# Optimization experiments

Hardware: AMD Instinct MI355X
Metric: run time of the kernel (lower is better)

Reference implementation:

```python
import jax, jax.numpy as jnp
import numpy as np

HID = 1024
HEADS = 16
HEAD_DIM = HID // HEADS
MLP_HID = 4096
TEMB = 1024
EPS = 1e-6


def _ln(x):
    # LayerNorm without affine, eps=1e-6
    mu = jnp.mean(x, axis=-1, keepdims=True)
    var = jnp.var(x, axis=-1, keepdims=True)
    return (x - mu) * jax.lax.rsqrt(var + EPS)


def _modulate(x, shift, scale):
    return x * (1.0 + scale[:, None, :]) + shift[:, None, :]


def setup_inputs() -> dict:
    key = jax.random.key(0)
    ks = jax.random.split(key, 12)
    s = 0.02
    return {
        "x": jax.random.normal(ks[0], (8, 1024, HID), jnp.float32),
        "c": jax.random.normal(ks[1], (8, TEMB), jnp.float32),
        "W_qkv": jax.random.normal(ks[2], (HID, 3 * HID), jnp.float32) * s,
        "b_qkv": jnp.zeros((3 * HID,), jnp.float32),
        "W_proj": jax.random.normal(ks[3], (HID, HID), jnp.float32) * s,
        "b_proj": jnp.zeros((HID,), jnp.float32),
        "W_fc1": jax.random.normal(ks[4], (HID, MLP_HID), jnp.float32) * s,
        "b_fc1": jnp.zeros((MLP_HID,), jnp.float32),
        "W_fc2": jax.random.normal(ks[5], (MLP_HID, HID), jnp.float32) * s,
        "b_fc2": jnp.zeros((HID,), jnp.float32),
        "W_ada": jax.random.normal(ks[6], (TEMB, 6 * HID), jnp.float32) * s,
        "b_ada": jnp.zeros((6 * HID,), jnp.float32),
    }


def _attn(x, W_qkv, b_qkv, W_proj, b_proj):
    B, N, C = x.shape
    qkv = x @ W_qkv + b_qkv                      # [B,N,3C]
    qkv = qkv.reshape(B, N, 3, HEADS, HEAD_DIM)
    q, k, v = qkv[:, :, 0], qkv[:, :, 1], qkv[:, :, 2]  # [B,N,H,D]
    scale = HEAD_DIM ** -0.5
    logits = jnp.einsum('bnhd,bmhd->bhnm', q, k) * scale
    attn = jax.nn.softmax(logits, axis=-1)
    out = jnp.einsum('bhnm,bmhd->bnhd', attn, v).reshape(B, N, C)
    return out @ W_proj + b_proj


def reference(x, c, W_qkv, b_qkv, W_proj, b_proj, W_fc1, b_fc1, W_fc2, b_fc2, W_ada, b_ada):
    ada = jax.nn.silu(c) @ W_ada + b_ada          # [B,6C]
    shift_msa, scale_msa, gate_msa, shift_mlp, scale_mlp, gate_mlp = jnp.split(ada, 6, axis=1)

    h = _modulate(_ln(x), shift_msa, scale_msa)
    x = x + gate_msa[:, None, :] * _attn(h, W_qkv, b_qkv, W_proj, b_proj)

    h = _modulate(_ln(x), shift_mlp, scale_mlp)
    h = jax.nn.gelu(h @ W_fc1 + b_fc1, approximate=True) @ W_fc2 + b_fc2
    x = x + gate_mlp[:, None, :] * h
    return x
```

## Files before the change

### kernel.cpp

```cpp
#include <hip/hip_runtime.h>
#include <stdint.h>

typedef unsigned short u16;
typedef __attribute__((ext_vector_type(4))) float f32x4;
typedef __attribute__((ext_vector_type(8))) short bf16x8;
typedef bf16x8 bf16x8a __attribute__((may_alias));
typedef uint32_t u32a __attribute__((may_alias));

#define HID 1024
#define MLPD 4096
#define TEMB 1024
#define ADA_N 6144
#define SEQ 1024
#define BATCH 8
#define KCH 32
#define KCHLEN (TEMB / KCH)

__device__ __forceinline__ u16 f2bf_bits(float f) {
  uint32_t u = __float_as_uint(f);
  uint32_t r = (u + 0x7FFFu + ((u >> 16) & 1u)) >> 16;
  return (u16)r;
}

__device__ __forceinline__ uint32_t cvt_pk_bf16(float lo, float hi) {
  uint32_t r;
  asm("v_cvt_pk_bf16_f32 %0, %1, %2" : "=v"(r) : "v"(lo), "v"(hi));
  return r;
}

__device__ __forceinline__ float exp2_hw(float x) {
#if __has_builtin(__builtin_amdgcn_exp2f)
  return __builtin_amdgcn_exp2f(x);
#else
  return exp2f(x);
#endif
}

__device__ __forceinline__ void async_copy16(void* lds_dst, const void* g_src) {
  __builtin_amdgcn_global_load_lds(
      (const __attribute__((address_space(1))) void*)(uintptr_t)g_src,
      (__attribute__((address_space(3))) void*)(uint32_t)(uintptr_t)lds_dst,
      16, 0, 0);
}

__device__ __forceinline__ float gelu_tanh(float v) {
  float u = 0.7978845608028654f * (v + 0.044715f * v * v * v);
  float e = __expf(2.f * u);
  return v * e / (e + 1.f);
}

__global__ __launch_bounds__(256) void transpose_bf16(const float* __restrict__ W,
                                                      u16* __restrict__ Wt, int K, int N) {
  __shared__ float tile[32][33];
  int n0 = blockIdx.x * 32, k0 = blockIdx.y * 32;
  int tx = threadIdx.x & 31, ty = threadIdx.x >> 5;
#pragma unroll
  for (int i = 0; i < 4; i++)
    tile[ty + i * 8][tx] = W[(size_t)(k0 + ty + i * 8) * N + n0 + tx];
  __syncthreads();
#pragma unroll
  for (int i = 0; i < 4; i++)
    Wt[(size_t)(n0 + ty + i * 8) * K + k0 + tx] = f2bf_bits(tile[tx][ty + i * 8]);
}

__global__ __launch_bounds__(256) void ada_part(const float* __restrict__ c,
                                                const float* __restrict__ W,
                                                float* __restrict__ part) {
  __shared__ float sc[BATCH * KCHLEN];
  int t = threadIdx.x;
  int col = blockIdx.x * 256 + t;
  int kc = blockIdx.y;
  int k0 = kc * KCHLEN;
  for (int i = t; i < BATCH * KCHLEN; i += 256) {
    int b = i >> 5, kk = i & (KCHLEN - 1);
    float v = c[b * TEMB + k0 + kk];
    sc[i] = v / (1.f + __expf(-v));
  }
  __syncthreads();
  float acc[BATCH] = {};
  for (int kk = 0; kk < KCHLEN; kk++) {
    float w = W[(size_t)(k0 + kk) * ADA_N + col];
#pragma unroll
    for (int b = 0; b < BATCH; b++) acc[b] += sc[b * KCHLEN + kk] * w;
  }
#pragma unroll
  for (int b = 0; b < BATCH; b++)
    part[((size_t)kc * BATCH + b) * ADA_N + col] = acc[b];
}

__global__ __launch_bounds__(256) void ada_reduce(const float* __restrict__ part,
                                                  const float* __restrict__ bias,
                                                  float* __restrict__ out) {
  int i = blockIdx.x * 256 + threadIdx.x;
  int col = i % ADA_N, b = i / ADA_N;
  float s = bias[col];
#pragma unroll
  for (int kc = 0; kc < KCH; kc++)
    s += part[((size_t)kc * BATCH + b) * ADA_N + col];
  out[(size_t)b * ADA_N + col] = s;
}

__global__ __launch_bounds__(256) void ln_mod(const float* __restrict__ x,
                                              const float* __restrict__ ada,
                                              int shift_off, int scale_off,
                                              u16* __restrict__ h) {
  int row = blockIdx.x;
  int bb = row >> 10;
  int t = threadIdx.x;
  const float4 v = ((const float4*)(x + (size_t)row * HID))[t];
  float s = v.x + v.y + v.z + v.w;
  float sq = v.x * v.x + v.y * v.y + v.z * v.z + v.w * v.w;
#pragma unroll
  for (int off = 32; off >= 1; off >>= 1) {
    s += __shfl_xor(s, off);
    sq += __shfl_xor(sq, off);
  }
  __shared__ float red[8];
  int wid = t >> 6;
  if ((t & 63) == 0) { red[wid] = s; red[4 + wid] = sq; }
  __syncthreads();
  s = red[0] + red[1] + red[2] + red[3];
  sq = red[4] + red[5] + red[6] + red[7];
  float mu = s * (1.0f / HID);
  float rs = rsqrtf(sq * (1.0f / HID) - mu * mu + 1e-6f);
  const float4 sc = ((const float4*)(ada + (size_t)bb * ADA_N + scale_off))[t];
  const float4 sh = ((const float4*)(ada + (size_t)bb * ADA_N + shift_off))[t];
  ushort4 o;
  o.x = f2bf_bits((v.x - mu) * rs * (1.f + sc.x) + sh.x);
  o.y = f2bf_bits((v.y - mu) * rs * (1.f + sc.y) + sh.y);
  o.z = f2bf_bits((v.z - mu) * rs * (1.f + sc.z) + sh.z);
  o.w = f2bf_bits((v.w - mu) * rs * (1.f + sc.w) + sh.w);
  ((ushort4*)(h + (size_t)row * HID))[t] = o;
}

template <int EPI>
__global__ __launch_bounds__(256) void gemm(const u16* __restrict__ A,
                                            const u16* __restrict__ Bt,
                                            const float* __restrict__ bias,
                                            void* __restrict__ Cout,
                                            const float* __restrict__ resid,
                                            const float* __restrict__ gate,
                                            int N, int K) {
  __shared__ u16 As[128 * 32];
  __shared__ u16 Bs[128 * 32];
  int t = threadIdx.x;
  int lane = t & 63, wid = t >> 6;
  int l15 = lane & 15, l4 = lane >> 4;
  int wr = wid >> 1, wc = wid & 1;
  int lid = blockIdx.y * gridDim.x + blockIdx.x;
  int nwg = gridDim.y * gridDim.x;
  int swz = (lid & 7) * (nwg >> 3) + (lid >> 3);
  int nx = gridDim.x;
  int m0 = (swz / nx) * 128, n0 = (swz % nx) * 128;
  f32x4 acc[4][4] = {};
  const u16* Abase = A + (size_t)m0 * K;
  const u16* Bbase = Bt + (size_t)n0 * K;
  for (int k0 = 0; k0 < K; k0 += 32) {
#pragma unroll
    for (int i = 0; i < 2; i++) {
      int idx = i * 256 + t;
      int row = idx >> 2, ch = idx & 3;
      async_copy16(&As[idx * 8], Abase + (size_t)row * K + k0 + ch * 8);
      async_copy16(&Bs[idx * 8], Bbase + (size_t)row * K + k0 + ch * 8);
    }
    asm volatile("s_waitcnt vmcnt(0)" ::: "memory");
    __syncthreads();
    bf16x8 af[4], bfr[4];
#pragma unroll
    for (int mi = 0; mi < 4; mi++)
      af[mi] = *(const bf16x8a*)&As[(wr * 64 + mi * 16 + l15) * 32 + l4 * 8];
#pragma unroll
    for (int ni = 0; ni < 4; ni++)
      bfr[ni] = *(const bf16x8a*)&Bs[(wc * 64 + ni * 16 + l15) * 32 + l4 * 8];
#pragma unroll
    for (int mi = 0; mi < 4; mi++)
#pragma unroll
      for (int ni = 0; ni < 4; ni++)
        acc[mi][ni] = __builtin_amdgcn_mfma_f32_16x16x32_bf16(af[mi], bfr[ni], acc[mi][ni], 0, 0, 0);
    __syncthreads();
  }
  int brow = m0 + wr * 64, bcol = n0 + wc * 64;
  int bb = m0 >> 10;
#pragma unroll
  for (int ni = 0; ni < 4; ni++) {
    int col = bcol + ni * 16 + l15;
    float bv = bias[col];
    float gv = (EPI == 2) ? gate[(size_t)bb * ADA_N + col] : 0.f;
#pragma unroll
    for (int mi = 0; mi < 4; mi++) {
#pragma unroll
      for (int r = 0; r < 4; r++) {
        int row = brow + mi * 16 + l4 * 4 + r;
        float v = acc[mi][ni][r] + bv;
        if (EPI == 0) {
          ((u16*)Cout)[(size_t)row * N + col] = f2bf_bits(v);
        } else if (EPI == 1) {
          ((u16*)Cout)[(size_t)row * N + col] = f2bf_bits(gelu_tanh(v));
        } else {
          ((float*)Cout)[(size_t)row * N + col] =
              resid[(size_t)row * N + col] + gv * v;
        }
      }
    }
  }
}

__global__ __launch_bounds__(256, 3) void attn_kernel(const u16* __restrict__ qkv,
                                                      u16* __restrict__ O) {
  const int KSTR = 72, VSTR = 72, PSTR = 72;
  __shared__ u16 Ks[64 * 72];
  __shared__ u16 Vt[64 * 72];
  __shared__ u16 Plds[4 * 16 * 72];
  int t = threadIdx.x, lane = t & 63, wid = t >> 6;
  int l15 = lane & 15, l4 = lane >> 4;
  int work = ((blockIdx.x & 7) << 7) + (blockIdx.x >> 3);
  int bh = work >> 3, qt8 = work & 7;
  int b = bh >> 4, h = bh & 15;
  int bRow = b * SEQ;
  int hOff = h * 64;
  int q0 = qt8 * 128 + wid * 32;

  bf16x8 qr[2][2];
#pragma unroll
  for (int qt = 0; qt < 2; qt++) {
    const u16* qbase = qkv + (size_t)(bRow + q0 + qt * 16 + l15) * 3072 + hOff;
    qr[qt][0] = *(const bf16x8a*)(qbase + l4 * 8);
    qr[qt][1] = *(const bf16x8a*)(qbase + 32 + l4 * 8);
  }

  const float csc = 0.125f * 1.4426950408889634f;
  float mrow[2] = {-1e30f, -1e30f};
  float lsum[2] = {0.f, 0.f};
  f32x4 o[2][4] = {};
  u16* pw = Plds + wid * 16 * PSTR;

  for (int cc = 0; cc < 16; cc++) {
    int kv0 = cc * 64;
    __syncthreads();
#pragma unroll
    for (int i = 0; i < 2; i++) {
      int idx = i * 256 + t;
      int row = idx >> 3, ch = idx & 7;
      bf16x8 kk = *(const bf16x8a*)(qkv + (size_t)(bRow + kv0 + row) * 3072 + 1024 + hOff + ch * 8);
      *(bf16x8a*)&Ks[row * KSTR + ch * 8] = kk;
    }
#pragma unroll
    for (int i = 0; i < 2; i++) {
      int idx = i * 256 + t;
      int kv = idx >> 3, dc = idx & 7;
      bf16x8 vv = *(const bf16x8a*)(qkv + (size_t)(bRow + kv0 + kv) * 3072 + 2048 + hOff + dc * 8);
#pragma unroll
      for (int j = 0; j < 8; j++) {
        int jj = (j + dc) & 7;
        Vt[(dc * 8 + jj) * VSTR + kv] = ((const u16*)&vv)[jj];
      }
    }
    __syncthreads();

    bf16x8 ak[4][2];
#pragma unroll
    for (int kt = 0; kt < 4; kt++) {
      ak[kt][0] = *(const bf16x8a*)&Ks[(kt * 16 + l15) * KSTR + l4 * 8];
      ak[kt][1] = *(const bf16x8a*)&Ks[(kt * 16 + l15) * KSTR + 32 + l4 * 8];
    }
    f32x4 st[2][4];
#pragma unroll
    for (int qt = 0; qt < 2; qt++)
#pragma unroll
      for (int kt = 0; kt < 4; kt++) {
        f32x4 z = {0.f, 0.f, 0.f, 0.f};
        z = __builtin_amdgcn_mfma_f32_16x16x32_bf16(ak[kt][0], qr[qt][0], z, 0, 0, 0);
        z = __builtin_amdgcn_mfma_f32_16x16x32_bf16(ak[kt][1], qr[qt][1], z, 0, 0, 0);
        st[qt][kt] = z;
      }
    bf16x8 av[4][2];
#pragma unroll
    for (int dt = 0; dt < 4; dt++) {
      av[dt][0] = *(const bf16x8a*)&Vt[(dt * 16 + l15) * VSTR + l4 * 8];
      av[dt][1] = *(const bf16x8a*)&Vt[(dt * 16 + l15) * VSTR + 32 + l4 * 8];
    }

#pragma unroll
    for (int qt = 0; qt < 2; qt++) {
      float mx = st[qt][0][0];
#pragma unroll
      for (int kt = 0; kt < 4; kt++)
#pragma unroll
        for (int r = 0; r < 4; r++) mx = fmaxf(mx, st[qt][kt][r]);
      mx = fmaxf(mx, __shfl_xor(mx, 16));
      mx = fmaxf(mx, __shfl_xor(mx, 32));
      float mn = fmaxf(mrow[qt], mx * csc);
      float al = exp2_hw(mrow[qt] - mn);
      mrow[qt] = mn;
      float rs = 0.f;
#pragma unroll
      for (int kt = 0; kt < 4; kt++)
#pragma unroll
        for (int r = 0; r < 4; r++) {
          float p = exp2_hw(__builtin_fmaf(st[qt][kt][r], csc, -mn));
          st[qt][kt][r] = p;
          rs += p;
        }
      rs += __shfl_xor(rs, 16);
      rs += __shfl_xor(rs, 32);
      lsum[qt] = lsum[qt] * al + rs;
#pragma unroll
      for (int dt = 0; dt < 4; dt++) o[qt][dt] *= al;
#pragma unroll
      for (int kt = 0; kt < 4; kt++) {
#pragma unroll
        for (int hh = 0; hh < 2; hh++) {
          uint32_t pk = cvt_pk_bf16(st[qt][kt][2 * hh], st[qt][kt][2 * hh + 1]);
          *(u32a*)&pw[l15 * PSTR + kt * 16 + l4 * 4 + 2 * hh] = pk;
        }
      }
      asm volatile("s_waitcnt lgkmcnt(0)" ::: "memory");
      __builtin_amdgcn_sched_barrier(0);
      bf16x8 bp0 = *(const bf16x8a*)&pw[l15 * PSTR + l4 * 8];
      bf16x8 bp1 = *(const bf16x8a*)&pw[l15 * PSTR + 32 + l4 * 8];
#pragma unroll
      for (int dt = 0; dt < 4; dt++) {
        o[qt][dt] = __builtin_amdgcn_mfma_f32_16x16x32_bf16(av[dt][0], bp0, o[qt][dt], 0, 0, 0);
        o[qt][dt] = __builtin_amdgcn_mfma_f32_16x16x32_bf16(av[dt][1], bp1, o[qt][dt], 0, 0, 0);
      }
      asm volatile("s_waitcnt lgkmcnt(0)" ::: "memory");
      __builtin_amdgcn_sched_barrier(0);
    }
  }
#pragma unroll
  for (int qt = 0; qt < 2; qt++) {
    float inv = 1.f / lsum[qt];
    u16* orow = O + (size_t)(bRow + q0 + qt * 16 + l15) * HID + hOff;
#pragma unroll
    for (int dt = 0; dt < 4; dt++) {
      uint2 w;
      w.x = cvt_pk_bf16(o[qt][dt][0] * inv, o[qt][dt][1] * inv);
      w.y = cvt_pk_bf16(o[qt][dt][2] * inv, o[qt][dt][3] * inv);
      *(uint2*)(orow + dt * 16 + l4 * 4) = w;
    }
  }
}

extern "C" void kernel_launch(void* const* d_in, const int* in_sizes, int n_in,
                              void* d_out, int out_size, void* d_ws, size_t ws_size,
                              hipStream_t stream) {
  const float* x      = (const float*)d_in[0];
  const float* c      = (const float*)d_in[1];
  const float* W_qkv  = (const float*)d_in[2];
  const float* b_qkv  = (const float*)d_in[3];
  const float* W_proj = (const float*)d_in[4];
  const float* b_proj = (const float*)d_in[5];
  const float* W_fc1  = (const float*)d_in[6];
  const float* b_fc1  = (const float*)d_in[7];
  const float* W_fc2  = (const float*)d_in[8];
  const float* b_fc2  = (const float*)d_in[9];
  const float* W_ada  = (const float*)d_in[10];
  const float* b_ada  = (const float*)d_in[11];
  float* out = (float*)d_out;
  char* ws = (char*)d_ws;

  float* ada  = (float*)(ws + 0);
  u16* WtQKV  = (u16*)(ws + 196608);
  u16* WtP    = (u16*)(ws + 6488064);
  u16* WtF1   = (u16*)(ws + 8585216);
  u16* WtF2   = (u16*)(ws + 16973824);
  u16* hbuf   = (u16*)(ws + 25362432);
  u16* big    = (u16*)(ws + 42139648);
  float* apart = (float*)(ws + 42139648);

  transpose_bf16<<<dim3(3072 / 32, 1024 / 32), 256, 0, stream>>>(W_qkv, WtQKV, 1024, 3072);
  transpose_bf16<<<dim3(1024 / 32, 1024 / 32), 256, 0, stream>>>(W_proj, WtP, 1024, 1024);
  transpose_bf16<<<dim3(4096 / 32, 1024 / 32), 256, 0, stream>>>(W_fc1, WtF1, 1024, 4096);
  transpose_bf16<<<dim3(1024 / 32, 4096 / 32), 256, 0, stream>>>(W_fc2, WtF2, 4096, 1024);
  ada_part<<<dim3(ADA_N / 256, KCH), 256, 0, stream>>>(c, W_ada, apart);
  ada_reduce<<<(BATCH * ADA_N) / 256, 256, 0, stream>>>(apart, b_ada, ada);
  ln_mod<<<8192, 256, 0, stream>>>(x, ada, 0, 1024, hbuf);
  gemm<0><<<dim3(3072 / 128, 8192 / 128), 256, 0, stream>>>(hbuf, WtQKV, b_qkv, big, nullptr, nullptr, 3072, 1024);
  attn_kernel<<<1024, 256, 0, stream>>>(big, hbuf);
  gemm<2><<<dim3(1024 / 128, 8192 / 128), 256, 0, stream>>>(hbuf, WtP, b_proj, out, x, ada + 2048, 1024, 1024);
  ln_mod<<<8192, 256, 0, stream>>>(out, ada, 3072, 4096, hbuf);
  gemm<1><<<dim3(4096 / 128, 8192 / 128), 256, 0, stream>>>(hbuf, WtF1, b_fc1, big, nullptr, nullptr, 4096, 1024);
  gemm<2><<<dim3(1024 / 128, 8192 / 128), 256, 0, stream>>>(big, WtF2, b_fc2, out, out, ada + 5120, 1024, 4096);
}
```

Before: 448.1 us.

## Double-buffer GEMM LDS tiles and remap workgroup tiles per XCD

Adds a second LDS buffer so the async global-to-LDS copy of the next K-slice is issued before the MFMA compute on the current slice, waiting only on the older loads via vmcnt(4). This overlaps memory latency with compute instead of serializing them. It also replaces the generic swizzle with a fixed mapping that assigns 8 consecutive M-tiles per XCD, aiming for better L2 reuse. The new mapping hardcodes a grid with 64 M-tiles (M=8192), which matches the problem but is fragile. LDS use doubles, which may lower occupancy.

```diff
diff --git a/kernel.cpp b/kernel.cpp
--- a/kernel.cpp
+++ b/kernel.cpp
@@ -133,6 +133,31 @@
   ((ushort4*)(h + (size_t)row * HID))[t] = o;
 }
 
+#define GEMM_STAGE(dA, dB, kk)                                              \
+  _Pragma("unroll")                                                         \
+  for (int i = 0; i < 2; i++) {                                             \
+    int idx = i * 256 + t;                                                  \
+    int row = idx >> 2, ch = idx & 3;                                       \
+    async_copy16(&(dA)[idx * 8], Abase + (size_t)row * K + (kk) + ch * 8);  \
+    async_copy16(&(dB)[idx * 8], Bbase + (size_t)row * K + (kk) + ch * 8);  \
+  }
+
+#define GEMM_COMPUTE(sA, sB)                                                \
+  {                                                                         \
+    bf16x8 af[4], bfr[4];                                                   \
+    _Pragma("unroll")                                                       \
+    for (int mi = 0; mi < 4; mi++)                                          \
+      af[mi] = *(const bf16x8a*)&(sA)[(wr * 64 + mi * 16 + l15) * 32 + l4 * 8]; \
+    _Pragma("unroll")                                                       \
+    for (int ni = 0; ni < 4; ni++)                                          \
+      bfr[ni] = *(const bf16x8a*)&(sB)[(wc * 64 + ni * 16 + l15) * 32 + l4 * 8]; \
+    _Pragma("unroll")                                                       \
+    for (int mi = 0; mi < 4; mi++)                                          \
+      _Pragma("unroll")                                                     \
+      for (int ni = 0; ni < 4; ni++)                                        \
+        acc[mi][ni] = __builtin_amdgcn_mfma_f32_16x16x32_bf16(af[mi], bfr[ni], acc[mi][ni], 0, 0, 0); \
+  }
+
 template <int EPI>
 __global__ __launch_bounds__(256) void gemm(const u16* __restrict__ A,
                                             const u16* __restrict__ Bt,
@@ -141,44 +166,39 @@
                                             const float* __restrict__ resid,
                                             const float* __restrict__ gate,
                                             int N, int K) {
-  __shared__ u16 As[128 * 32];
-  __shared__ u16 Bs[128 * 32];
+  __shared__ u16 As0[128 * 32], As1[128 * 32];
+  __shared__ u16 Bs0[128 * 32], Bs1[128 * 32];
   int t = threadIdx.x;
   int lane = t & 63, wid = t >> 6;
   int l15 = lane & 15, l4 = lane >> 4;
   int wr = wid >> 1, wc = wid & 1;
   int lid = blockIdx.y * gridDim.x + blockIdx.x;
-  int nwg = gridDim.y * gridDim.x;
-  int swz = (lid & 7) * (nwg >> 3) + (lid >> 3);
-  int nx = gridDim.x;
-  int m0 = (swz / nx) * 128, n0 = (swz % nx) * 128;
+  int xcd = lid & 7, within = lid >> 3;
+  int m0 = (xcd * 8 + (within & 7)) * 128;
+  int n0 = (within >> 3) * 128;
   f32x4 acc[4][4] = {};
   const u16* Abase = A + (size_t)m0 * K;
   const u16* Bbase = Bt + (size_t)n0 * K;
-  for (int k0 = 0; k0 < K; k0 += 32) {
-#pragma unroll
-    for (int i = 0; i < 2; i++) {
-      int idx = i * 256 + t;
-      int row = idx >> 2, ch = idx & 3;
-      async_copy16(&As[idx * 8], Abase + (size_t)row * K + k0 + ch * 8);
-      async_copy16(&Bs[idx * 8], Bbase + (size_t)row * K + k0 + ch * 8);
-    }
-    asm volatile("s_waitcnt vmcnt(0)" ::: "memory");
-    __syncthreads();
-    bf16x8 af[4], bfr[4];
-#pragma unroll
-    for (int mi = 0; mi < 4; mi++)
-      af[mi] = *(const bf16x8a*)&As[(wr * 64 + mi * 16 + l15) * 32 + l4 * 8];
-#pragma unroll
-    for (int ni = 0; ni < 4; ni++)
-      bfr[ni] = *(const bf16x8a*)&Bs[(wc * 64 + ni * 16 + l15) * 32 + l4 * 8];
-#pragma unroll
-    for (int mi = 0; mi < 4; mi++)
-#pragma unroll
-      for (int ni = 0; ni < 4; ni++)
-        acc[mi][ni] = __builtin_amdgcn_mfma_f32_16x16x32_bf16(af[mi], bfr[ni], acc[mi][ni], 0, 0, 0);
-    __syncthreads();
-  }
+
+  u16 *cA = As0, *cB = Bs0, *nA = As1, *nB = Bs1;
+  GEMM_STAGE(cA, cB, 0)
+  int nt = K / 32;
+  for (int ts = 0; ts < nt - 1; ++ts) {
+    int k1 = (ts + 1) * 32;
+    GEMM_STAGE(nA, nB, k1)
+    asm volatile("s_waitcnt vmcnt(4)" ::: "memory");
+    __builtin_amdgcn_s_barrier();
+    GEMM_COMPUTE(cA, cB)
+    asm volatile("" ::: "memory");
+    __builtin_amdgcn_s_barrier();
+    u16* tp;
+    tp = cA; cA = nA; nA = tp;
+    tp = cB; cB = nB; nB = tp;
+  }
+  asm volatile("s_waitcnt vmcnt(0)" ::: "memory");
+  __builtin_amdgcn_s_barrier();
+  GEMM_COMPUTE(cA, cB)
+
   int brow = m0 + wr * 64, bcol = n0 + wc * 64;
   int bb = m0 >> 10;
 #pragma unroll
```

Result: faster. 421.1 us (-6.0%).

## Replace GEMM with double-buffered 256-row tile kernel using swizzled LDS

Applied to the files above, without the earlier changes.

Replaces the 128x128, K=32 single-buffered GEMM with a 512-thread kernel that uses 256xBN tiles, K=64 steps, and double-buffered async global-to-LDS staging. An XOR swizzle on the LDS layout avoids bank conflicts, and the grid is remapped so neighbouring row blocks land on the same XCD. Wave priority boosting and explicit barriers are meant to overlap loads with MFMA work and to raise arithmetic intensity per byte loaded. The larger LDS footprint and register count reduce occupancy, and the fixed grid sizes bake in the problem shape.

```diff
diff --git a/kernel.cpp b/kernel.cpp
--- a/kernel.cpp
+++ b/kernel.cpp
@@ -133,63 +133,117 @@
   ((ushort4*)(h + (size_t)row * HID))[t] = o;
 }
 
-template <int EPI>
-__global__ __launch_bounds__(256) void gemm(const u16* __restrict__ A,
-                                            const u16* __restrict__ Bt,
-                                            const float* __restrict__ bias,
-                                            void* __restrict__ Cout,
-                                            const float* __restrict__ resid,
-                                            const float* __restrict__ gate,
-                                            int N, int K) {
-  __shared__ u16 As[128 * 32];
-  __shared__ u16 Bs[128 * 32];
+
+template <int NLOAD>
+__device__ __forceinline__ void stage_tile(u16* dst, const u16* gsrc, int K, int koff, int t) {
+#pragma unroll
+  for (int i = 0; i < NLOAD; ++i) {
+    int slot = i * 512 + t;
+    int row = slot >> 3, cp = slot & 7;
+    const u16* src = gsrc + (size_t)row * K + koff + ((cp ^ (row & 7)) << 3);
+    async_copy16(dst + slot * 8, src);
+  }
+}
+
+#define LDSRD(buf, row, kk) \
+  (*(const bf16x8a*)&(buf)[(row) * 64 + ((((kk) * 4 + l4) ^ ((row) & 7)) << 3)])
+
+template <int EPI, int BN>
+__global__ __launch_bounds__(512, 2) void gemm8(const u16* __restrict__ A,
+                                                const u16* __restrict__ Bt,
+                                                const float* __restrict__ bias,
+                                                void* __restrict__ Cout,
+                                                const float* __restrict__ resid,
+                                                const float* __restrict__ gate,
+                                                int N, int K) {
+  constexpr int NR = BN / 64;
+  constexpr int BLOADS = BN / 64;
+  constexpr int TOT = 4 + BLOADS;
+  __shared__ u16 As[2][256 * 64];
+  __shared__ u16 Bs[2][BN * 64];
+
   int t = threadIdx.x;
   int lane = t & 63, wid = t >> 6;
   int l15 = lane & 15, l4 = lane >> 4;
-  int wr = wid >> 1, wc = wid & 1;
-  int lid = blockIdx.y * gridDim.x + blockIdx.x;
-  int nwg = gridDim.y * gridDim.x;
-  int swz = (lid & 7) * (nwg >> 3) + (lid >> 3);
-  int nx = gridDim.x;
-  int m0 = (swz / nx) * 128, n0 = (swz % nx) * 128;
-  f32x4 acc[4][4] = {};
+  int wr = wid >> 2, wc = wid & 3;
+  int lid = blockIdx.x;
+  int xcd = lid & 7, win = lid >> 3;
+  int m0 = (xcd * 4 + (win & 3)) * 256;
+  int n0 = (win >> 2) * BN;
+
   const u16* Abase = A + (size_t)m0 * K;
   const u16* Bbase = Bt + (size_t)n0 * K;
-  for (int k0 = 0; k0 < K; k0 += 32) {
-#pragma unroll
-    for (int i = 0; i < 2; i++) {
-      int idx = i * 256 + t;
-      int row = idx >> 2, ch = idx & 3;
-      async_copy16(&As[idx * 8], Abase + (size_t)row * K + k0 + ch * 8);
-      async_copy16(&Bs[idx * 8], Bbase + (size_t)row * K + k0 + ch * 8);
-    }
-    asm volatile("s_waitcnt vmcnt(0)" ::: "memory");
-    __syncthreads();
-    bf16x8 af[4], bfr[4];
-#pragma unroll
-    for (int mi = 0; mi < 4; mi++)
-      af[mi] = *(const bf16x8a*)&As[(wr * 64 + mi * 16 + l15) * 32 + l4 * 8];
-#pragma unroll
-    for (int ni = 0; ni < 4; ni++)
-      bfr[ni] = *(const bf16x8a*)&Bs[(wc * 64 + ni * 16 + l15) * 32 + l4 * 8];
-#pragma unroll
-    for (int mi = 0; mi < 4; mi++)
-#pragma unroll
-      for (int ni = 0; ni < 4; ni++)
-        acc[mi][ni] = __builtin_amdgcn_mfma_f32_16x16x32_bf16(af[mi], bfr[ni], acc[mi][ni], 0, 0, 0);
-    __syncthreads();
-  }
-  int brow = m0 + wr * 64, bcol = n0 + wc * 64;
+  f32x4 acc[8][NR] = {};
+
+  u16 *cA = As[0], *cB = Bs[0], *nA = As[1], *nB = Bs[1];
+  int nt = K / 64;
+  stage_tile<4>(cA, Abase, K, 0, t);
+  stage_tile<BLOADS>(cB, Bbase, K, 0, t);
+  stage_tile<4>(nA, Abase, K, 64, t);
+  stage_tile<BLOADS>(nB, Bbase, K, 64, t);
+  if constexpr (TOT == 8) asm volatile("s_waitcnt vmcnt(8)" ::: "memory");
+  else                    asm volatile("s_waitcnt vmcnt(6)" ::: "memory");
+  __builtin_amdgcn_s_barrier();
+  __builtin_amdgcn_sched_barrier(0);
+
+  for (int ts = 0; ts < nt; ++ts) {
+    bf16x8 bf[NR][2];
+#pragma unroll
+    for (int p = 0; p < 4; ++p) {
+      if (p == 0) {
+#pragma unroll
+        for (int ni = 0; ni < NR; ++ni)
+#pragma unroll
+          for (int kk = 0; kk < 2; ++kk)
+            bf[ni][kk] = LDSRD(cB, wc * (16 * NR) + ni * 16 + l15, kk);
+      }
+      bf16x8 af[2][2];
+#pragma unroll
+      for (int i = 0; i < 2; ++i)
+#pragma unroll
+        for (int kk = 0; kk < 2; ++kk)
+          af[i][kk] = LDSRD(cA, wr * 128 + (p * 2 + i) * 16 + l15, kk);
+      asm volatile("s_waitcnt lgkmcnt(0)" ::: "memory");
+      __builtin_amdgcn_sched_barrier(0);
+      __builtin_amdgcn_s_setprio(1);
+#pragma unroll
+      for (int i = 0; i < 2; ++i)
+#pragma unroll
+        for (int ni = 0; ni < NR; ++ni) {
+          acc[p * 2 + i][ni] = __builtin_amdgcn_mfma_f32_16x16x32_bf16(af[i][0], bf[ni][0], acc[p * 2 + i][ni], 0, 0, 0);
+          acc[p * 2 + i][ni] = __builtin_amdgcn_mfma_f32_16x16x32_bf16(af[i][1], bf[ni][1], acc[p * 2 + i][ni], 0, 0, 0);
+        }
+      __builtin_amdgcn_s_setprio(0);
+      __builtin_amdgcn_sched_barrier(0);
+      __builtin_amdgcn_s_barrier();
+      __builtin_amdgcn_sched_barrier(0);
+    }
+    if (ts + 2 < nt) {
+      stage_tile<4>(cA, Abase, K, (ts + 2) * 64, t);
+      stage_tile<BLOADS>(cB, Bbase, K, (ts + 2) * 64, t);
+      if constexpr (TOT == 8) asm volatile("s_waitcnt vmcnt(8)" ::: "memory");
+      else                    asm volatile("s_waitcnt vmcnt(6)" ::: "memory");
+    } else if (ts + 1 < nt) {
+      asm volatile("s_waitcnt vmcnt(0)" ::: "memory");
+    }
+    __builtin_amdgcn_s_barrier();
+    __builtin_amdgcn_sched_barrier(0);
+    u16* tp;
+    tp = cA; cA = nA; nA = tp;
+    tp = cB; cB = nB; nB = tp;
+  }
+
+  int brow = m0 + wr * 128, bcol = n0 + wc * (16 * NR);
   int bb = m0 >> 10;
 #pragma unroll
-  for (int ni = 0; ni < 4; ni++) {
+  for (int ni = 0; ni < NR; ++ni) {
     int col = bcol + ni * 16 + l15;
     float bv = bias[col];
     float gv = (EPI == 2) ? gate[(size_t)bb * ADA_N + col] : 0.f;
 #pragma unroll
-    for (int mi = 0; mi < 4; mi++) {
-#pragma unroll
-      for (int r = 0; r < 4; r++) {
+    for (int mi = 0; mi < 8; ++mi) {
+#pragma unroll
+      for (int r = 0; r < 4; ++r) {
         int row = brow + mi * 16 + l4 * 4 + r;
         float v = acc[mi][ni][r] + bv;
         if (EPI == 0) {
@@ -375,10 +429,10 @@
   ada_part<<<dim3(ADA_N / 256, KCH), 256, 0, stream>>>(c, W_ada, apart);
   ada_reduce<<<(BATCH * ADA_N) / 256, 256, 0, stream>>>(apart, b_ada, ada);
   ln_mod<<<8192, 256, 0, stream>>>(x, ada, 0, 1024, hbuf);
-  gemm<0><<<dim3(3072 / 128, 8192 / 128), 256, 0, stream>>>(hbuf, WtQKV, b_qkv, big, nullptr, nullptr, 3072, 1024);
+  gemm8<0, 128><<<768, 512, 0, stream>>>(hbuf, WtQKV, b_qkv, big, nullptr, nullptr, 3072, 1024);
   attn_kernel<<<1024, 256, 0, stream>>>(big, hbuf);
-  gemm<2><<<dim3(1024 / 128, 8192 / 128), 256, 0, stream>>>(hbuf, WtP, b_proj, out, x, ada + 2048, 1024, 1024);
+  gemm8<2, 128><<<256, 512, 0, stream>>>(hbuf, WtP, b_proj, out, x, ada + 2048, 1024, 1024);
   ln_mod<<<8192, 256, 0, stream>>>(out, ada, 3072, 4096, hbuf);
-  gemm<1><<<dim3(4096 / 128, 8192 / 128), 256, 0, stream>>>(hbuf, WtF1, b_fc1, big, nullptr, nullptr, 4096, 1024);
-  gemm<2><<<dim3(1024 / 128, 8192 / 128), 256, 0, stream>>>(big, WtF2, b_fc2, out, out, ada + 5120, 1024, 4096);
-}
+  gemm8<1, 256><<<512, 512, 0, stream>>>(hbuf, WtF1, b_fc1, big, nullptr, nullptr, 4096, 1024);
+  gemm8<2, 128><<<256, 512, 0, stream>>>(big, WtF2, b_fc2, out, out, ada + 5120, 1024, 4096);
+}
```

After: 405.1 us, median of 2. 1.11x faster.
